# Performance work log

Measured on AMD Instinct MI355X. Metric: run time of the kernel, lower is better.

The kernel has to match this reference:

```python
import jax, jax.numpy as jnp
import numpy as np

HIDDEN = 512
NUM_HEADS = 8
HEAD = HIDDEN // NUM_HEADS
TOP_K = 64
NEG = -1e9


def setup_inputs() -> dict:
    key = jax.random.key(0)
    ks = jax.random.split(key, 12)
    B, Q, S = 2, 2048, 4096
    sc = 0.02
    return {
        "main_input": jax.random.normal(ks[0], (B, Q, HIDDEN), jnp.float32),
        "side_input": jax.random.normal(ks[1], (S, HIDDEN), jnp.float32),
        "att_mask": jax.random.randint(ks[2], (B, Q, S), 0, 2, jnp.int32),
        "Wq": jax.random.normal(ks[3], (HIDDEN, HIDDEN), jnp.float32) * sc,
        "bq": jnp.zeros((HIDDEN,), jnp.float32),
        "Wk": jax.random.normal(ks[4], (HIDDEN, HIDDEN), jnp.float32) * sc,
        "bk": jnp.zeros((HIDDEN,), jnp.float32),
        "Wv": jax.random.normal(ks[5], (HIDDEN, HIDDEN), jnp.float32) * sc,
        "bv": jnp.zeros((HIDDEN,), jnp.float32),
        "Wo": jax.random.normal(ks[6], (HIDDEN, HIDDEN), jnp.float32) * sc,
        "bo": jnp.zeros((HIDDEN,), jnp.float32),
    }


def reference(main_input, side_input, att_mask, Wq, bq, Wk, bk, Wv, bv, Wo, bo):
    B, Qlen, _ = main_input.shape
    S = side_input.shape[0]
    # multi-head projections; side K/V shared across the whole batch
    q = (main_input @ Wq + bq).reshape(B, Qlen, NUM_HEADS, HEAD)
    k = (side_input @ Wk + bk).reshape(S, NUM_HEADS, HEAD)
    v = (side_input @ Wv + bv).reshape(S, NUM_HEADS, HEAD)
    # scores: [B, H, Q, S]
    scores = jnp.einsum("bqhd,khd->bhqk", q, k) / jnp.sqrt(jnp.asarray(HEAD, q.dtype))
    # attention mask (0 = masked)
    mask = att_mask[:, None, :, :].astype(scores.dtype)  # [B,1,Q,S]
    scores = scores + (1.0 - mask) * NEG
    # top-k restriction: keep only the TOP_K largest scores per query row
    thresh = jax.lax.top_k(scores, TOP_K)[0][..., -1:]  # kth largest
    scores = jnp.where(scores >= thresh, scores, NEG)
    probs = jax.nn.softmax(scores, axis=-1)
    ctx = jnp.einsum("bhqk,khd->bqhd", probs, v).reshape(B, Qlen, HIDDEN)
    return ctx @ Wo + bo
```

## Files before the change

kernel.cpp:

```cpp
#include <hip/hip_runtime.h>
#include <stdint.h>

typedef uint32_t u32;
typedef unsigned long long u64;

#define NEGV (-1e9f)
#define MAXSEL 128
#define NCAND 16

__device__ __forceinline__ u32 f2ord(float f) {
  u32 x = __float_as_uint(f);
  return (x & 0x80000000u) ? ~x : (x | 0x80000000u);
}
__device__ __forceinline__ float ord2f(u32 u) {
  u32 x = (u & 0x80000000u) ? (u ^ 0x80000000u) : ~u;
  return __uint_as_float(x);
}

__global__ __launch_bounds__(256)
void pack_mask(const int* __restrict__ mask, u64* __restrict__ mbits) {
  int w = blockIdx.x * 256 + threadIdx.x;
  const int4* p = (const int4*)(mask + (size_t)w * 64);
  u64 bits = 0;
#pragma unroll
  for (int j = 0; j < 16; ++j) {
    int4 m = p[j];
    if (m.x) bits |= 1ull << (j * 4 + 0);
    if (m.y) bits |= 1ull << (j * 4 + 1);
    if (m.z) bits |= 1ull << (j * 4 + 2);
    if (m.w) bits |= 1ull << (j * 4 + 3);
  }
  mbits[w] = bits;
}

__global__ __launch_bounds__(256)
void gemm_bias(const float* __restrict__ A, const float* __restrict__ W,
               const float* __restrict__ bias, float* __restrict__ C) {
  __shared__ float As[16][68];
  __shared__ float Bs[16][64];
  const int tid = threadIdx.x;
  const int tx = tid & 15, ty = tid >> 4;
  const int n0 = blockIdx.x << 6, m0 = blockIdx.y << 6;
  float c[4][4] = {};
  for (int k0 = 0; k0 < 512; k0 += 16) {
    {
      const int row = tid >> 2, kp = (tid & 3) << 2;
      float4 av = *(const float4*)&A[(size_t)(m0 + row) * 512 + k0 + kp];
      As[kp + 0][row] = av.x;
      As[kp + 1][row] = av.y;
      As[kp + 2][row] = av.z;
      As[kp + 3][row] = av.w;
      const int kk = tid >> 4, np = (tid & 15) << 2;
      *(float4*)&Bs[kk][np] = *(const float4*)&W[(size_t)(k0 + kk) * 512 + n0 + np];
    }
    __syncthreads();
#pragma unroll
    for (int kk = 0; kk < 16; ++kk) {
      float4 a = *(const float4*)&As[kk][ty << 2];
      float4 b = *(const float4*)&Bs[kk][tx << 2];
      c[0][0] += a.x * b.x; c[0][1] += a.x * b.y; c[0][2] += a.x * b.z; c[0][3] += a.x * b.w;
      c[1][0] += a.y * b.x; c[1][1] += a.y * b.y; c[1][2] += a.y * b.z; c[1][3] += a.y * b.w;
      c[2][0] += a.z * b.x; c[2][1] += a.z * b.y; c[2][2] += a.z * b.z; c[2][3] += a.z * b.w;
      c[3][0] += a.w * b.x; c[3][1] += a.w * b.y; c[3][2] += a.w * b.z; c[3][3] += a.w * b.w;
    }
    __syncthreads();
  }
  float4 bv = *(const float4*)&bias[n0 + (tx << 2)];
#pragma unroll
  for (int i = 0; i < 4; ++i) {
    float4 o;
    o.x = c[i][0] + bv.x; o.y = c[i][1] + bv.y;
    o.z = c[i][2] + bv.z; o.w = c[i][3] + bv.w;
    *(float4*)&C[(size_t)(m0 + (ty << 2) + i) * 512 + n0 + (tx << 2)] = o;
  }
}

__global__ __launch_bounds__(256)
void gemm_bias_T(const float* __restrict__ A, const float* __restrict__ W,
                 const float* __restrict__ bias, float* __restrict__ CT, int qsh) {
  __shared__ float As[16][68];
  __shared__ float Bs[16][64];
  const int tid = threadIdx.x;
  const int tx = tid & 15, ty = tid >> 4;
  const int n0 = blockIdx.x << 6, m0 = blockIdx.y << 6;
  float c[4][4] = {};
  for (int k0 = 0; k0 < 512; k0 += 16) {
    {
      const int row = tid >> 2, kp = (tid & 3) << 2;
      float4 av = *(const float4*)&A[(size_t)(m0 + row) * 512 + k0 + kp];
      As[kp + 0][row] = av.x;
      As[kp + 1][row] = av.y;
      As[kp + 2][row] = av.z;
      As[kp + 3][row] = av.w;
      const int kk = tid >> 4, np = (tid & 15) << 2;
      *(float4*)&Bs[kk][np] = *(const float4*)&W[(size_t)(k0 + kk) * 512 + n0 + np];
    }
    __syncthreads();
#pragma unroll
    for (int kk = 0; kk < 16; ++kk) {
      float4 a = *(const float4*)&As[kk][ty << 2];
      float4 b = *(const float4*)&Bs[kk][tx << 2];
      c[0][0] += a.x * b.x; c[0][1] += a.x * b.y; c[0][2] += a.x * b.z; c[0][3] += a.x * b.w;
      c[1][0] += a.y * b.x; c[1][1] += a.y * b.y; c[1][2] += a.y * b.z; c[1][3] += a.y * b.w;
      c[2][0] += a.z * b.x; c[2][1] += a.z * b.y; c[2][2] += a.z * b.z; c[2][3] += a.z * b.w;
      c[3][0] += a.w * b.x; c[3][1] += a.w * b.y; c[3][2] += a.w * b.z; c[3][3] += a.w * b.w;
    }
    __syncthreads();
  }
  float4 bv = *(const float4*)&bias[n0 + (tx << 2)];
  float bvv[4] = {bv.x, bv.y, bv.z, bv.w};
  const int qlen = 1 << qsh;
  const int qmask = qlen - 1;
#pragma unroll
  for (int i = 0; i < 4; ++i) {
#pragma unroll
    for (int j = 0; j < 4; ++j) {
      float val = c[i][j] + bvv[j];
      int m = m0 + (ty << 2) + i;
      int n = n0 + (tx << 2) + j;
      int h = n >> 6, d = n & 63;
      int bb = m >> qsh, q = m & qmask;
      CT[(((size_t)bb * 8 + h) * 64 + d) * qlen + q] = val;
    }
  }
}

__global__ __launch_bounds__(256)
void score_kernel(const float* __restrict__ qT, const float* __restrict__ kT,
                  const u64* __restrict__ mbits, float* __restrict__ sbuf, int sl0) {
  __shared__ float Qs[64][128];
  __shared__ float Ks[64][128];
  const int sl = sl0 + blockIdx.z;
  const int b = sl >> 3, h = sl & 7;
  const int s0 = blockIdx.x << 7, q0 = blockIdx.y << 7;
  const int tid = threadIdx.x;
  const float* qbase = qT + (size_t)sl * 64 * 2048 + q0;
  const float* kbase = kT + (size_t)h * 64 * 4096 + s0;
  float4* Qf = (float4*)&Qs[0][0];
  float4* Kf = (float4*)&Ks[0][0];
#pragma unroll
  for (int u = 0; u < 8; ++u) {
    int i = (u << 8) + tid;
    int row = i >> 5, col = (i & 31) << 2;
    Qf[i] = *(const float4*)(qbase + (size_t)row * 2048 + col);
    Kf[i] = *(const float4*)(kbase + (size_t)row * 4096 + col);
  }
  __syncthreads();
  const int tx = tid & 15, ty = tid >> 4;
  float c[8][8] = {};
#pragma unroll 4
  for (int g = 0; g < 16; ++g) {
    const int kk = g << 2;
    float qa[8][4], kb[8][4];
#pragma unroll
    for (int t = 0; t < 4; ++t) {
#pragma unroll
      for (int i = 0; i < 8; ++i) qa[i][t] = Qs[kk + t][(ty << 3) + i];
#pragma unroll
      for (int j = 0; j < 4; ++j) {
        kb[j][t]     = Ks[kk + t][(tx << 2) + j];
        kb[4 + j][t] = Ks[kk + t][64 + (tx << 2) + j];
      }
    }
#pragma unroll
    for (int i = 0; i < 8; ++i)
#pragma unroll
      for (int j = 0; j < 8; ++j)
        c[i][j] += qa[i][0] * kb[j][0] + qa[i][1] * kb[j][1]
                 + qa[i][2] * kb[j][2] + qa[i][3] * kb[j][3];
  }
  float* srow = sbuf + ((size_t)blockIdx.z * 2048 + q0) * 4096 + s0;
  const u64* mrow = mbits + ((size_t)(b * 2048 + q0)) * 64 + (s0 >> 6);
#pragma unroll
  for (int i = 0; i < 8; ++i) {
    const int row = (ty << 3) + i;
    u64 wA = mrow[(size_t)row * 64];
    u64 wB = mrow[(size_t)row * 64 + 1];
    float4 o0, o1;
    o0.x = ((wA >> ((tx << 2) + 0)) & 1) ? c[i][0] * 0.125f : NEGV;
    o0.y = ((wA >> ((tx << 2) + 1)) & 1) ? c[i][1] * 0.125f : NEGV;
    o0.z = ((wA >> ((tx << 2) + 2)) & 1) ? c[i][2] * 0.125f : NEGV;
    o0.w = ((wA >> ((tx << 2) + 3)) & 1) ? c[i][3] * 0.125f : NEGV;
    o1.x = ((wB >> ((tx << 2) + 0)) & 1) ? c[i][4] * 0.125f : NEGV;
    o1.y = ((wB >> ((tx << 2) + 1)) & 1) ? c[i][5] * 0.125f : NEGV;
    o1.z = ((wB >> ((tx << 2) + 2)) & 1) ? c[i][6] * 0.125f : NEGV;
    o1.w = ((wB >> ((tx << 2) + 3)) & 1) ? c[i][7] * 0.125f : NEGV;
    *(float4*)&srow[(size_t)row * 4096 + (tx << 2)] = o0;
    *(float4*)&srow[(size_t)row * 4096 + 64 + (tx << 2)] = o1;
  }
}

__global__ __launch_bounds__(64, 2)
void select_kernel(const float* __restrict__ sbuf, const float* __restrict__ vbuf,
                   float* __restrict__ ctxbuf, int sl0) {
  const int sl = sl0 + blockIdx.y;
  const int b = sl >> 3, h = sl & 7;
  const int qi = blockIdx.x;
  const int lane = threadIdx.x;
  __shared__ u32 cv_lds[NCAND][64];
  __shared__ u64 list[MAXSEL];

  const float* srow = sbuf + ((size_t)blockIdx.y * 2048 + qi) * 4096;
  const u32 ordneg = f2ord(NEGV);
  const u64 lmask_lt = (1ull << lane) - 1ull;

  u32 u[64];
#pragma unroll
  for (int j = 0; j < 16; ++j) {
    float4 v = *(const float4*)(srow + (j << 8) + (lane << 2));
    u[j * 4 + 0] = f2ord(v.x);
    u[j * 4 + 1] = f2ord(v.y);
    u[j * 4 + 2] = f2ord(v.z);
    u[j * 4 + 3] = f2ord(v.w);
  }
  u32 lmax = 0;
#pragma unroll
  for (int e = 0; e < 64; ++e) lmax = u[e] > lmax ? u[e] : lmax;
  u32 mx = lmax, mn = lmax;
#pragma unroll
  for (int off = 32; off; off >>= 1) {
    u32 a = (u32)__shfl_xor((int)mx, off, 64);
    u32 c = (u32)__shfl_xor((int)mn, off, 64);
    mx = a > mx ? a : mx;
    mn = c < mn ? c : mn;
  }
  const float fm = ord2f(mx);
  const u32 lo0 = mn;

  int cnt = 0;
#pragma unroll
  for (int e = 0; e < 64; ++e) {
    u32 ue = u[e];
    if (ue >= lo0 && ue != ordneg) {
      if (cnt < NCAND) cv_lds[cnt][lane] = ue;
      cnt++;
    }
  }
  const bool fb = (__ballot(cnt > NCAND) != 0ull);

  u32 lo = lo0, hi = mx + 1;
  if (!fb) {
#pragma unroll
    for (int j = 0; j < NCAND; ++j)
      if (j >= cnt) cv_lds[j][lane] = 0;
    u32 cv[NCAND];
#pragma unroll
    for (int j = 0; j < NCAND; ++j) cv[j] = cv_lds[j][lane];
    while (hi - lo > 1) {
      u32 mid = lo + ((hi - lo) >> 1);
      int c2 = 0;
#pragma unroll
      for (int j = 0; j < NCAND; ++j)
        c2 += __popcll(__ballot(cv[j] >= mid));
      if (c2 >= 64) lo = mid; else hi = mid;
    }
  } else {
    while (hi - lo > 1) {
      u32 mid = lo + ((hi - lo) >> 1);
      int c2 = 0;
#pragma unroll
      for (int e = 0; e < 64; ++e)
        c2 += __popcll(__ballot(u[e] >= mid));
      if (c2 >= 64) lo = mid; else hi = mid;
    }
  }
  const u32 thr = lo;

  float esum = 0.f;
  int base = 0;
#pragma unroll
  for (int e = 0; e < 64; ++e) {
    u32 ue = u[e];
    bool pred = (ue >= thr) && (ue != ordneg);
    float ev = __expf(ord2f(ue) - fm);
    u64 m = __ballot(pred);
    int ofs = base + __popcll(m & lmask_lt);
    if (pred && ofs < MAXSEL) {
      int sidx = ((e >> 2) << 8) + (lane << 2) + (e & 3);
      list[ofs] = ((u64)(u32)sidx << 32) | (u64)__float_as_uint(ev);
      esum += ev;
    }
    base += (int)__popcll(m);
  }
  int nsel = base < MAXSEL ? base : MAXSEL;
  int pad = (4 - (nsel & 3)) & 3;
  if (lane < pad && nsel + lane < MAXSEL) list[nsel + lane] = 0;
  int n4 = nsel + pad;
  if (n4 > MAXSEL) n4 = MAXSEL;

#pragma unroll
  for (int off = 32; off; off >>= 1) esum += __shfl_xor(esum, off, 64);
  const float rs = 1.0f / esum;

  const float* vb = vbuf + h * 64 + lane;
  float a0 = 0.f, a1 = 0.f, a2 = 0.f, a3 = 0.f;
  for (int g = 0; g < n4; g += 4) {
    u64 p0 = list[g + 0], p1 = list[g + 1], p2 = list[g + 2], p3 = list[g + 3];
    a0 += __uint_as_float((u32)p0) * vb[(size_t)(p0 >> 32) * 512];
    a1 += __uint_as_float((u32)p1) * vb[(size_t)(p1 >> 32) * 512];
    a2 += __uint_as_float((u32)p2) * vb[(size_t)(p2 >> 32) * 512];
    a3 += __uint_as_float((u32)p3) * vb[(size_t)(p3 >> 32) * 512];
  }
  float acc = (a0 + a1) + (a2 + a3);
  ctxbuf[((size_t)(b * 2048 + qi)) * 512 + h * 64 + lane] = acc * rs;
}

extern "C" void kernel_launch(void* const* d_in, const int* in_sizes, int n_in,
                              void* d_out, int out_size, void* d_ws, size_t ws_size,
                              hipStream_t stream) {
  const float* main_in = (const float*)d_in[0];
  const float* side_in = (const float*)d_in[1];
  const int*   mask    = (const int*)d_in[2];
  const float* Wq = (const float*)d_in[3];
  const float* bq = (const float*)d_in[4];
  const float* Wk = (const float*)d_in[5];
  const float* bk = (const float*)d_in[6];
  const float* Wv = (const float*)d_in[7];
  const float* bv = (const float*)d_in[8];
  const float* Wo = (const float*)d_in[9];
  const float* bo = (const float*)d_in[10];
  float* out = (float*)d_out;

  char* ws = (char*)d_ws;
  float* qT   = (float*)(ws);
  float* kT   = (float*)(ws + ((size_t)8 << 20));
  float* vbuf = (float*)(ws + ((size_t)16 << 20));
  float* ctxb = (float*)(ws + ((size_t)24 << 20));
  u64* mbits  = (u64*)(ws + ((size_t)32 << 20));
  float* sbuf = (float*)(ws + ((size_t)34 << 20));
  const size_t base = (size_t)34 << 20;
  const size_t sliceb = (size_t)2048 * 4096 * 4;

  int nz = 1;
  if (ws_size > base + sliceb) {
    size_t m = (ws_size - base) / sliceb;
    nz = (int)(m > 16 ? 16 : m);
  }

  pack_mask<<<1024, 256, 0, stream>>>(mask, mbits);
  gemm_bias_T<<<dim3(8, 64), 256, 0, stream>>>(main_in, Wq, bq, qT, 11);
  gemm_bias_T<<<dim3(8, 64), 256, 0, stream>>>(side_in, Wk, bk, kT, 12);
  gemm_bias  <<<dim3(8, 64), 256, 0, stream>>>(side_in, Wv, bv, vbuf);

  for (int sl0 = 0; sl0 < 16; sl0 += nz) {
    int z = nz < (16 - sl0) ? nz : (16 - sl0);
    score_kernel <<<dim3(32, 16, z), 256, 0, stream>>>(qT, kT, mbits, sbuf, sl0);
    select_kernel<<<dim3(2048, z), 64, 0, stream>>>(sbuf, vbuf, ctxb, sl0);
  }

  gemm_bias<<<dim3(8, 64), 256, 0, stream>>>(ctxb, Wo, bo, out);
}
```

Before: 860.7 us.

## Split top-k selection into candidate filter and finish kernels

Replaces the single per-row select kernel with two kernels. A filter kernel compacts candidates (scores at or above the min of per-lane maxima) into a global buffer. A finish kernel runs the threshold bisection over at most 256 candidates held in registers, then does the softmax and the V gather with 8-way unrolling. The aim is to cut register pressure and the per-row 64-element ballot work, and to raise occupancy by using 256-thread blocks with four rows each. In exchange it adds a global round trip for candidates, and a slow fallback that rereads the score row when there are too many candidates.

```diff
diff --git a/kernel.cpp b/kernel.cpp
--- a/kernel.cpp
+++ b/kernel.cpp
@@ -5,8 +5,8 @@
 typedef unsigned long long u64;
 
 #define NEGV (-1e9f)
-#define MAXSEL 128
-#define NCAND 16
+#define CAP 256
+#define SENTINEL 0xFFFFFFFFu
 
 __device__ __forceinline__ u32 f2ord(float f) {
   u32 x = __float_as_uint(f);
@@ -190,119 +190,191 @@
   }
 }
 
-__global__ __launch_bounds__(64, 2)
-void select_kernel(const float* __restrict__ sbuf, const float* __restrict__ vbuf,
+__global__ __launch_bounds__(256)
+void filter_kernel(const float* __restrict__ sbuf, u64* __restrict__ cand,
+                   u32* __restrict__ hdr) {
+  const int w = threadIdx.x >> 6, lane = threadIdx.x & 63;
+  const int qi = (blockIdx.x << 2) + w;
+  const float* srow = sbuf + ((size_t)blockIdx.y * 2048 + qi) * 4096;
+  u64* crow = cand + ((size_t)blockIdx.y * 2048 + qi) * CAP;
+  const u64 lmask_lt = (1ull << lane) - 1ull;
+
+  float f[64];
+#pragma unroll
+  for (int j = 0; j < 16; ++j) {
+    float4 v = *(const float4*)(srow + (j << 8) + (lane << 2));
+    f[j * 4 + 0] = v.x; f[j * 4 + 1] = v.y;
+    f[j * 4 + 2] = v.z; f[j * 4 + 3] = v.w;
+  }
+  float lmax = f[0];
+#pragma unroll
+  for (int e = 1; e < 64; ++e) lmax = fmaxf(lmax, f[e]);
+  float mn = lmax;
+#pragma unroll
+  for (int off = 32; off; off >>= 1) mn = fminf(mn, __shfl_xor(mn, off, 64));
+  const float lo0f = mn;
+
+  int base = 0;
+#pragma unroll
+  for (int e = 0; e < 64; ++e) {
+    bool pred = f[e] >= lo0f;
+    u64 m = __ballot(pred);
+    if (m != 0ull) {
+      int ofs = base + __popcll(m & lmask_lt);
+      if (pred && ofs < CAP) {
+        int sidx = ((e >> 2) << 8) + (lane << 2) + (e & 3);
+        crow[ofs] = ((u64)f2ord(f[e]) << 32) | (u32)sidx;
+      }
+      base += (int)__popcll(m);
+    }
+  }
+  if (lane == 0) hdr[blockIdx.y * 2048 + qi] = (base <= CAP) ? (u32)base : SENTINEL;
+}
+
+__global__ __launch_bounds__(256)
+void finish_kernel(const float* __restrict__ sbuf, const u64* __restrict__ cand,
+                   const u32* __restrict__ hdr, const float* __restrict__ vbuf,
                    float* __restrict__ ctxbuf, int sl0) {
   const int sl = sl0 + blockIdx.y;
   const int b = sl >> 3, h = sl & 7;
-  const int qi = blockIdx.x;
-  const int lane = threadIdx.x;
-  __shared__ u32 cv_lds[NCAND][64];
-  __shared__ u64 list[MAXSEL];
-
-  const float* srow = sbuf + ((size_t)blockIdx.y * 2048 + qi) * 4096;
+  const int w = threadIdx.x >> 6, lane = threadIdx.x & 63;
+  const int qi = (blockIdx.x << 2) + w;
+  __shared__ u64 list_s[4][CAP + 8];
+  u64* list = list_s[w];
+  const u64 lmask_lt = (1ull << lane) - 1ull;
   const u32 ordneg = f2ord(NEGV);
-  const u64 lmask_lt = (1ull << lane) - 1ull;
-
-  u32 u[64];
-#pragma unroll
-  for (int j = 0; j < 16; ++j) {
-    float4 v = *(const float4*)(srow + (j << 8) + (lane << 2));
-    u[j * 4 + 0] = f2ord(v.x);
-    u[j * 4 + 1] = f2ord(v.y);
-    u[j * 4 + 2] = f2ord(v.z);
-    u[j * 4 + 3] = f2ord(v.w);
-  }
-  u32 lmax = 0;
-#pragma unroll
-  for (int e = 0; e < 64; ++e) lmax = u[e] > lmax ? u[e] : lmax;
-  u32 mx = lmax, mn = lmax;
-#pragma unroll
-  for (int off = 32; off; off >>= 1) {
-    u32 a = (u32)__shfl_xor((int)mx, off, 64);
-    u32 c = (u32)__shfl_xor((int)mn, off, 64);
-    mx = a > mx ? a : mx;
-    mn = c < mn ? c : mn;
-  }
-  const float fm = ord2f(mx);
-  const u32 lo0 = mn;
-
-  int cnt = 0;
-#pragma unroll
-  for (int e = 0; e < 64; ++e) {
-    u32 ue = u[e];
-    if (ue >= lo0 && ue != ordneg) {
-      if (cnt < NCAND) cv_lds[cnt][lane] = ue;
-      cnt++;
-    }
-  }
-  const bool fb = (__ballot(cnt > NCAND) != 0ull);
-
-  u32 lo = lo0, hi = mx + 1;
-  if (!fb) {
-#pragma unroll
-    for (int j = 0; j < NCAND; ++j)
-      if (j >= cnt) cv_lds[j][lane] = 0;
-    u32 cv[NCAND];
-#pragma unroll
-    for (int j = 0; j < NCAND; ++j) cv[j] = cv_lds[j][lane];
+
+  const u32 cnt = hdr[blockIdx.y * 2048 + qi];
+  float esum = 0.f;
+  int nsel = 0;
+  bool meanpath = false;
+
+  if (cnt != SENTINEL) {
+    const u64* crow = cand + ((size_t)blockIdx.y * 2048 + qi) * CAP;
+    u64 c0 = crow[lane * 4 + 0], c1 = crow[lane * 4 + 1];
+    u64 c2 = crow[lane * 4 + 2], c3 = crow[lane * 4 + 3];
+    u32 n = lane * 4;
+    if (n + 0 >= cnt) c0 = 0;
+    if (n + 1 >= cnt) c1 = 0;
+    if (n + 2 >= cnt) c2 = 0;
+    if (n + 3 >= cnt) c3 = 0;
+    u64 mx = c0 > c1 ? c0 : c1;
+    u64 t = c2 > c3 ? c2 : c3;
+    mx = mx > t ? mx : t;
+    u64 z0 = c0 ? c0 : ~0ull, z1 = c1 ? c1 : ~0ull;
+    u64 z2 = c2 ? c2 : ~0ull, z3 = c3 ? c3 : ~0ull;
+    u64 mnp = z0 < z1 ? z0 : z1;
+    u64 t2 = z2 < z3 ? z2 : z3;
+    mnp = mnp < t2 ? mnp : t2;
+#pragma unroll
+    for (int off = 32; off; off >>= 1) {
+      u64 a = (u64)__shfl_xor((long long)mx, off, 64);
+      u64 bb = (u64)__shfl_xor((long long)mnp, off, 64);
+      mx = a > mx ? a : mx;
+      mnp = bb < mnp ? bb : mnp;
+    }
+    u32 lo = (u32)(mnp >> 32), hi = (u32)(mx >> 32) + 1;
     while (hi - lo > 1) {
       u32 mid = lo + ((hi - lo) >> 1);
-      int c2 = 0;
-#pragma unroll
-      for (int j = 0; j < NCAND; ++j)
-        c2 += __popcll(__ballot(cv[j] >= mid));
-      if (c2 >= 64) lo = mid; else hi = mid;
-    }
+      u64 mp = (u64)mid << 32;
+      int c = __popcll(__ballot(c0 >= mp)) + __popcll(__ballot(c1 >= mp)) +
+              __popcll(__ballot(c2 >= mp)) + __popcll(__ballot(c3 >= mp));
+      if (c >= 64) lo = mid; else hi = mid;
+    }
+    const float fm = ord2f((u32)(mx >> 32));
+    const u64 tp = (u64)lo << 32;
+    int base = 0;
+    u64 cj[4] = {c0, c1, c2, c3};
+#pragma unroll
+    for (int j = 0; j < 4; ++j) {
+      bool pred = cj[j] >= tp;
+      u64 m = __ballot(pred);
+      int ofs = base + __popcll(m & lmask_lt);
+      if (pred && ofs < CAP) {
+        float ev = __expf(ord2f((u32)(cj[j] >> 32)) - fm);
+        list[ofs] = ((u64)((u32)cj[j]) << 32) | (u64)__float_as_uint(ev);
+        esum += ev;
+      }
+      base += (int)__popcll(m);
+    }
+    nsel = base < CAP ? base : CAP;
   } else {
+    const float* srow = sbuf + ((size_t)blockIdx.y * 2048 + qi) * 4096;
+    float lmax = NEGV;
+#pragma unroll
+    for (int j = 0; j < 16; ++j) {
+      float4 v = *(const float4*)(srow + (j << 8) + (lane << 2));
+      lmax = fmaxf(fmaxf(fmaxf(lmax, v.x), fmaxf(v.y, v.z)), v.w);
+    }
+#pragma unroll
+    for (int off = 32; off; off >>= 1) lmax = fmaxf(lmax, __shfl_xor(lmax, off, 64));
+    const float fm = lmax;
+    u32 lo = ordneg, hi = f2ord(fm) + 1;
     while (hi - lo > 1) {
       u32 mid = lo + ((hi - lo) >> 1);
-      int c2 = 0;
-#pragma unroll
-      for (int e = 0; e < 64; ++e)
-        c2 += __popcll(__ballot(u[e] >= mid));
-      if (c2 >= 64) lo = mid; else hi = mid;
-    }
-  }
-  const u32 thr = lo;
-
-  float esum = 0.f;
-  int base = 0;
-#pragma unroll
-  for (int e = 0; e < 64; ++e) {
-    u32 ue = u[e];
-    bool pred = (ue >= thr) && (ue != ordneg);
-    float ev = __expf(ord2f(ue) - fm);
-    u64 m = __ballot(pred);
-    int ofs = base + __popcll(m & lmask_lt);
-    if (pred && ofs < MAXSEL) {
-      int sidx = ((e >> 2) << 8) + (lane << 2) + (e & 3);
-      list[ofs] = ((u64)(u32)sidx << 32) | (u64)__float_as_uint(ev);
-      esum += ev;
-    }
-    base += (int)__popcll(m);
-  }
-  int nsel = base < MAXSEL ? base : MAXSEL;
-  int pad = (4 - (nsel & 3)) & 3;
-  if (lane < pad && nsel + lane < MAXSEL) list[nsel + lane] = 0;
-  int n4 = nsel + pad;
-  if (n4 > MAXSEL) n4 = MAXSEL;
+      float midf = ord2f(mid);
+      int c = 0;
+      for (int j = 0; j < 16; ++j) {
+        float4 v = *(const float4*)(srow + (j << 8) + (lane << 2));
+        c += __popcll(__ballot(v.x >= midf)) + __popcll(__ballot(v.y >= midf)) +
+             __popcll(__ballot(v.z >= midf)) + __popcll(__ballot(v.w >= midf));
+      }
+      if (c >= 64) lo = mid; else hi = mid;
+    }
+    const float thrf = ord2f(lo);
+    int base = 0;
+    for (int j = 0; j < 16; ++j) {
+      float4 v = *(const float4*)(srow + (j << 8) + (lane << 2));
+      float xs[4] = {v.x, v.y, v.z, v.w};
+#pragma unroll
+      for (int cpos = 0; cpos < 4; ++cpos) {
+        float x = xs[cpos];
+        bool pred = (x >= thrf) && (x != NEGV);
+        u64 m = __ballot(pred);
+        int ofs = base + __popcll(m & lmask_lt);
+        if (pred && ofs < CAP) {
+          int sidx = (j << 8) + (lane << 2) + cpos;
+          float ev = __expf(x - fm);
+          list[ofs] = ((u64)(u32)sidx << 32) | (u64)__float_as_uint(ev);
+          esum += ev;
+        }
+        base += (int)__popcll(m);
+      }
+    }
+    nsel = base < CAP ? base : CAP;
+    if (base == 0) meanpath = true;
+  }
 
 #pragma unroll
   for (int off = 32; off; off >>= 1) esum += __shfl_xor(esum, off, 64);
-  const float rs = 1.0f / esum;
-
   const float* vb = vbuf + h * 64 + lane;
-  float a0 = 0.f, a1 = 0.f, a2 = 0.f, a3 = 0.f;
-  for (int g = 0; g < n4; g += 4) {
-    u64 p0 = list[g + 0], p1 = list[g + 1], p2 = list[g + 2], p3 = list[g + 3];
-    a0 += __uint_as_float((u32)p0) * vb[(size_t)(p0 >> 32) * 512];
-    a1 += __uint_as_float((u32)p1) * vb[(size_t)(p1 >> 32) * 512];
-    a2 += __uint_as_float((u32)p2) * vb[(size_t)(p2 >> 32) * 512];
-    a3 += __uint_as_float((u32)p3) * vb[(size_t)(p3 >> 32) * 512];
-  }
-  float acc = (a0 + a1) + (a2 + a3);
-  ctxbuf[((size_t)(b * 2048 + qi)) * 512 + h * 64 + lane] = acc * rs;
+  float outv;
+  if (!meanpath) {
+    const float rs = 1.0f / esum;
+    int pad = (8 - (nsel & 7)) & 7;
+    if (lane < pad) list[nsel + lane] = 0;
+    int n8 = nsel + pad;
+    float a0 = 0.f, a1 = 0.f, a2 = 0.f, a3 = 0.f;
+    float a4 = 0.f, a5 = 0.f, a6 = 0.f, a7 = 0.f;
+    for (int g = 0; g < n8; g += 8) {
+      u64 p0 = list[g + 0], p1 = list[g + 1], p2 = list[g + 2], p3 = list[g + 3];
+      u64 p4 = list[g + 4], p5 = list[g + 5], p6 = list[g + 6], p7 = list[g + 7];
+      a0 += __uint_as_float((u32)p0) * vb[(size_t)(p0 >> 32) * 512];
+      a1 += __uint_as_float((u32)p1) * vb[(size_t)(p1 >> 32) * 512];
+      a2 += __uint_as_float((u32)p2) * vb[(size_t)(p2 >> 32) * 512];
+      a3 += __uint_as_float((u32)p3) * vb[(size_t)(p3 >> 32) * 512];
+      a4 += __uint_as_float((u32)p4) * vb[(size_t)(p4 >> 32) * 512];
+      a5 += __uint_as_float((u32)p5) * vb[(size_t)(p5 >> 32) * 512];
+      a6 += __uint_as_float((u32)p6) * vb[(size_t)(p6 >> 32) * 512];
+      a7 += __uint_as_float((u32)p7) * vb[(size_t)(p7 >> 32) * 512];
+    }
+    outv = (((a0 + a1) + (a2 + a3)) + ((a4 + a5) + (a6 + a7))) * rs;
+  } else {
+    float acc = 0.f;
+    for (int s = 0; s < 4096; ++s) acc += vb[(size_t)s * 512];
+    outv = acc * (1.0f / 4096.0f);
+  }
+  ctxbuf[((size_t)(b * 2048 + qi)) * 512 + h * 64 + lane] = outv;
 }
 
 extern "C" void kernel_launch(void* const* d_in, const int* in_sizes, int n_in,
@@ -327,15 +399,20 @@
   float* vbuf = (float*)(ws + ((size_t)16 << 20));
   float* ctxb = (float*)(ws + ((size_t)24 << 20));
   u64* mbits  = (u64*)(ws + ((size_t)32 << 20));
-  float* sbuf = (float*)(ws + ((size_t)34 << 20));
   const size_t base = (size_t)34 << 20;
   const size_t sliceb = (size_t)2048 * 4096 * 4;
+  const size_t candb  = (size_t)2048 * CAP * 8;
+  const size_t hdrb   = (size_t)64 << 10;
+  const size_t per = sliceb + candb + hdrb;
 
   int nz = 1;
-  if (ws_size > base + sliceb) {
-    size_t m = (ws_size - base) / sliceb;
+  if (ws_size > base + per) {
+    size_t m = (ws_size - base) / per;
     nz = (int)(m > 16 ? 16 : m);
   }
+  float* sbuf = (float*)(ws + base);
+  u64*   cand = (u64*)(ws + base + (size_t)nz * sliceb);
+  u32*   hdr  = (u32*)(ws + base + (size_t)nz * (sliceb + candb));
 
   pack_mask<<<1024, 256, 0, stream>>>(mask, mbits);
   gemm_bias_T<<<dim3(8, 64), 256, 0, stream>>>(main_in, Wq, bq, qT, 11);
@@ -345,7 +422,8 @@
   for (int sl0 = 0; sl0 < 16; sl0 += nz) {
     int z = nz < (16 - sl0) ? nz : (16 - sl0);
     score_kernel <<<dim3(32, 16, z), 256, 0, stream>>>(qT, kT, mbits, sbuf, sl0);
-    select_kernel<<<dim3(2048, z), 64, 0, stream>>>(sbuf, vbuf, ctxb, sl0);
+    filter_kernel<<<dim3(512, z), 256, 0, stream>>>(sbuf, cand, hdr);
+    finish_kernel<<<dim3(512, z), 256, 0, stream>>>(sbuf, cand, hdr, vbuf, ctxb, sl0);
   }
 
   gemm_bias<<<dim3(8, 64), 256, 0, stream>>>(ctxb, Wo, bo, out);
```

Result: slower. 2.242 ms (+160.5%).
